# Optimization experiments

Hardware: AMD Instinct MI355X
Metric: run time of the kernel (lower is better)

Reference implementation:

```python
import jax, jax.numpy as jnp
import numpy as np

BS = 128  # quantization block size


def _dequant(w, s, bs):
    # w: [E, O, I]; s: [E, O//bs, I//bs] block scales -> broadcast to full weight
    return w * jnp.repeat(jnp.repeat(s, bs, axis=1), bs, axis=2)


def setup_inputs() -> dict:
    key = jax.random.key(0)
    ks = jax.random.split(key, 9)
    T, H, I, E, K = 512, 2048, 1024, 16, 4
    x = jax.random.normal(ks[0], (T, H), dtype=jnp.float32)
    w0 = jax.random.normal(ks[1], (E, I, H), dtype=jnp.float32) * 0.02
    w1 = jax.random.normal(ks[2], (E, I, H), dtype=jnp.float32) * 0.02
    w2 = jax.random.normal(ks[3], (E, H, I), dtype=jnp.float32) * 0.02
    s0 = jax.random.uniform(ks[4], (E, I // BS, H // BS), dtype=jnp.float32) + 0.5
    s1 = jax.random.uniform(ks[5], (E, I // BS, H // BS), dtype=jnp.float32) + 0.5
    s2 = jax.random.uniform(ks[6], (E, H // BS, I // BS), dtype=jnp.float32) + 0.5
    selected_experts = jax.random.randint(ks[7], (T, K), 0, E, dtype=jnp.int64)
    routing_weights = jax.random.uniform(ks[8], (T, K), dtype=jnp.float32)
    return {"x": x, "w0": w0, "w1": w1, "w2": w2, "s0": s0, "s1": s1,
            "s2": s2, "selected_experts": selected_experts,
            "routing_weights": routing_weights}


def reference(x, w0, w1, w2, s0, s1, s2, selected_experts, routing_weights):
    # Dequantize block-quantized expert weights
    w0d = _dequant(w0, s0, BS)  # [E, I, H] gate proj
    w1d = _dequant(w1, s1, BS)  # [E, I, H] up proj
    w2d = _dequant(w2, s2, BS)  # [E, H, I] down proj
    # SwiGLU FFN for every (token, expert) pair via batched GEMMs
    g = jnp.einsum('th,eih->tei', x, w0d)          # [T, E, I]
    u = jnp.einsum('th,eih->tei', x, w1d)          # [T, E, I]
    h = jax.nn.silu(g) * u                          # [T, E, I]
    y = jnp.einsum('tei,ehi->teh', h, w2d)          # [T, E, H]
    # Gather the top-k selected experts per token and weight them
    idx = selected_experts[:, :, None]              # [T, K, 1]
    y_sel = jnp.take_along_axis(y, idx, axis=1)     # [T, K, H]
    out = y_sel * routing_weights[:, :, None]       # [T, K, H]
    return out
```

## Files before the change

### kernel.cpp

```cpp
#include <hip/hip_runtime.h>
#include <math.h>

#define T_DIM 512
#define H_DIM 2048
#define I_DIM 1024
#define E_DIM 16
#define NP    2048
#define BM    64
#define MAXCH 48
#define LIST_OFF 256
#define HWS_OFF  4096
#define BK    128
#define LDK   136

typedef float  float4v __attribute__((ext_vector_type(4)));
typedef short  short8v __attribute__((ext_vector_type(8)));

__device__ __forceinline__ unsigned int bfr(float f) {
    unsigned int u = __builtin_bit_cast(unsigned int, f);
    return (u + 0x7fffu + ((u >> 16) & 1u)) >> 16;
}
__device__ __forceinline__ unsigned int cvt2(float a, float b) {
    unsigned int r;
    asm("v_cvt_pk_bf16_f32 %0, %1, %2" : "=v"(r) : "v"(a), "v"(b));
    return r;
}

__global__ __launch_bounds__(1024) void route_kernel(const int* __restrict__ sel,
                                                     int* __restrict__ meta) {
    __shared__ int cnt[E_DIM];
    __shared__ int wptr[E_DIM];
    int tid = threadIdx.x;
    if (tid < E_DIM) cnt[tid] = 0;
    __syncthreads();
    int p0 = tid, p1 = tid + 1024;
    int e0 = sel[p0], e1 = sel[p1];
    atomicAdd(&cnt[e0], 1);
    atomicAdd(&cnt[e1], 1);
    for (int i = tid; i < MAXCH * BM; i += 1024) meta[LIST_OFF + i] = -1;
    __syncthreads();
    if (tid == 0) {
        int off = 0, ci = 0;
        for (int e = 0; e < E_DIM; ++e) {
            wptr[e] = off;
            int nch = (cnt[e] + BM - 1) / BM;
            for (int j = 0; j < nch; ++j) meta[32 + ci++] = e;
            off += nch * BM;
        }
        for (; ci < MAXCH; ++ci) meta[32 + ci] = -1;
    }
    __syncthreads();
    int pos0 = atomicAdd(&wptr[e0], 1);
    meta[LIST_OFF + pos0] = p0;
    int pos1 = atomicAdd(&wptr[e1], 1);
    meta[LIST_OFF + pos1] = p1;
}

__global__ __launch_bounds__(512, 4) void gemm01_kernel(
    const float* __restrict__ x, const float* __restrict__ w0g,
    const float* __restrict__ w1g, const float* __restrict__ s0,
    const float* __restrict__ s1, const int* __restrict__ meta,
    unsigned short* __restrict__ hbuf) {
    int e = meta[32 + blockIdx.y];
    if (e < 0) return;
    int itile = blockIdx.x;
    int tid = threadIdx.x;

    __shared__ unsigned short xs[BM][LDK];
    __shared__ unsigned short as[BM][LDK];
    __shared__ unsigned short bs[BM][LDK];
    __shared__ int prow[BM];
    __shared__ int trow[BM];

    if (tid < BM) {
        int p = meta[LIST_OFF + blockIdx.y * BM + tid];
        prow[tid] = p;
        trow[tid] = p >= 0 ? (p >> 2) : 0;
    }
    __syncthreads();

    const int lane = tid & 63;
    const int wid  = tid >> 6;
    const int wm   = wid & 3;
    const int wn   = wid >> 2;
    const int l15  = lane & 15;
    const int kq   = (lane >> 4) * 8;
    const int ib   = itile >> 1;

    float4v zero = {0.f, 0.f, 0.f, 0.f};
    float4v accg[2], accu[2];
    accg[0] = accg[1] = accu[0] = accu[1] = zero;

    const int r  = tid >> 3;
    const int c0 = tid & 7;
    const float* xrow  = x   + (size_t)trow[r] * H_DIM;
    const float* w0row = w0g + ((size_t)e * I_DIM + itile * 64 + r) * H_DIM;
    const float* w1row = w1g + ((size_t)e * I_DIM + itile * 64 + r) * H_DIM;
    const float* s0p = s0 + ((size_t)e * (I_DIM/128) + ib) * (H_DIM/128);
    const float* s1p = s1 + ((size_t)e * (I_DIM/128) + ib) * (H_DIM/128);

    float4 px[4], pa[4], pb[4];
#pragma unroll
    for (int q = 0; q < 4; ++q) {
        int c4 = (c0 + q * 8) * 4;
        px[q] = *(const float4*)(xrow + c4);
        pa[q] = *(const float4*)(w0row + c4);
        pb[q] = *(const float4*)(w1row + c4);
    }

    for (int hb = 0; hb < H_DIM / BK; ++hb) {
        float sg = s0p[hb];
        float su = s1p[hb];
#pragma unroll
        for (int q = 0; q < 4; ++q) {
            int c4 = (c0 + q * 8) * 4;
            *(uint2*)&xs[r][c4] = make_uint2(cvt2(px[q].x, px[q].y), cvt2(px[q].z, px[q].w));
            *(uint2*)&as[r][c4] = make_uint2(cvt2(pa[q].x * sg, pa[q].y * sg),
                                             cvt2(pa[q].z * sg, pa[q].w * sg));
            *(uint2*)&bs[r][c4] = make_uint2(cvt2(pb[q].x * su, pb[q].y * su),
                                             cvt2(pb[q].z * su, pb[q].w * su));
        }
        __syncthreads();
        if (hb + 1 < H_DIM / BK) {
            const int h0 = (hb + 1) * BK;
#pragma unroll
            for (int q = 0; q < 4; ++q) {
                int c4 = (c0 + q * 8) * 4;
                px[q] = *(const float4*)(xrow + h0 + c4);
                pa[q] = *(const float4*)(w0row + h0 + c4);
                pb[q] = *(const float4*)(w1row + h0 + c4);
            }
        }
#pragma unroll
        for (int ks = 0; ks < BK / 32; ++ks) {
            int koff = ks * 32 + kq;
            short8v af = *(const short8v*)&xs[wm * 16 + l15][koff];
#pragma unroll
            for (int nt = 0; nt < 2; ++nt) {
                short8v b0 = *(const short8v*)&as[wn * 32 + nt * 16 + l15][koff];
                accg[nt] = __builtin_amdgcn_mfma_f32_16x16x32_bf16(af, b0, accg[nt], 0, 0, 0);
                short8v b1 = *(const short8v*)&bs[wn * 32 + nt * 16 + l15][koff];
                accu[nt] = __builtin_amdgcn_mfma_f32_16x16x32_bf16(af, b1, accu[nt], 0, 0, 0);
            }
        }
        __syncthreads();
    }

    int rowb = wm * 16 + (lane >> 4) * 4;
    int colb = itile * 64 + wn * 32 + l15;
#pragma unroll
    for (int nt = 0; nt < 2; ++nt) {
#pragma unroll
        for (int rg = 0; rg < 4; ++rg) {
            int p = prow[rowb + rg];
            if (p < 0) continue;
            float g = accg[nt][rg], u = accu[nt][rg];
            float h = g / (1.f + __expf(-g)) * u;
            hbuf[(size_t)p * I_DIM + colb + nt * 16] = (unsigned short)bfr(h);
        }
    }
}

__global__ __launch_bounds__(512, 4) void gemm2_kernel(
    const unsigned short* __restrict__ hbuf, const float* __restrict__ w2g,
    const float* __restrict__ s2, const float* __restrict__ rw,
    const int* __restrict__ meta, float* __restrict__ out) {
    int e = meta[32 + blockIdx.y];
    if (e < 0) return;
    int htile = blockIdx.x;
    int tid = threadIdx.x;

    __shared__ unsigned short hs[BM][LDK];
    __shared__ unsigned short wsm[BM][LDK];
    __shared__ int prow[BM];

    if (tid < BM) prow[tid] = meta[LIST_OFF + blockIdx.y * BM + tid];
    __syncthreads();

    const int lane = tid & 63;
    const int wid  = tid >> 6;
    const int wm   = wid & 3;
    const int wn   = wid >> 2;
    const int l15  = lane & 15;
    const int kq   = (lane >> 4) * 8;
    const int hbk  = htile >> 1;

    float4v zero = {0.f, 0.f, 0.f, 0.f};
    float4v acc[2];
    acc[0] = acc[1] = zero;

    const int r  = tid >> 3;
    const int c0 = tid & 7;
    int pr = prow[r]; if (pr < 0) pr = 0;
    const unsigned short* hrow = hbuf + (size_t)pr * I_DIM;
    const float* wrow = w2g + ((size_t)e * H_DIM + htile * 64 + r) * I_DIM;
    const float* s2p = s2 + ((size_t)e * (H_DIM/128) + hbk) * (I_DIM/128);

    uint2  ph[4];
    float4 pw[4];
#pragma unroll
    for (int q = 0; q < 4; ++q) {
        int c4 = (c0 + q * 8) * 4;
        ph[q] = *(const uint2*)(hrow + c4);
        pw[q] = *(const float4*)(wrow + c4);
    }

    for (int ibk = 0; ibk < I_DIM / BK; ++ibk) {
        float sc = s2p[ibk];
#pragma unroll
        for (int q = 0; q < 4; ++q) {
            int c4 = (c0 + q * 8) * 4;
            *(uint2*)&hs[r][c4] = ph[q];
            *(uint2*)&wsm[r][c4] = make_uint2(cvt2(pw[q].x * sc, pw[q].y * sc),
                                              cvt2(pw[q].z * sc, pw[q].w * sc));
        }
        __syncthreads();
        if (ibk + 1 < I_DIM / BK) {
            const int i0 = (ibk + 1) * BK;
#pragma unroll
            for (int q = 0; q < 4; ++q) {
                int c4 = (c0 + q * 8) * 4;
                ph[q] = *(const uint2*)(hrow + i0 + c4);
                pw[q] = *(const float4*)(wrow + i0 + c4);
            }
        }
#pragma unroll
        for (int ks = 0; ks < BK / 32; ++ks) {
            int koff = ks * 32 + kq;
            short8v af = *(const short8v*)&hs[wm * 16 + l15][koff];
#pragma unroll
            for (int nt = 0; nt < 2; ++nt) {
                short8v bfv = *(const short8v*)&wsm[wn * 32 + nt * 16 + l15][koff];
                acc[nt] = __builtin_amdgcn_mfma_f32_16x16x32_bf16(af, bfv, acc[nt], 0, 0, 0);
            }
        }
        __syncthreads();
    }

    int rowb = wm * 16 + (lane >> 4) * 4;
    int colb = htile * 64 + wn * 32 + l15;
#pragma unroll
    for (int nt = 0; nt < 2; ++nt) {
#pragma unroll
        for (int rg = 0; rg < 4; ++rg) {
            int p = prow[rowb + rg];
            if (p < 0) continue;
            out[(size_t)p * H_DIM + colb + nt * 16] = acc[nt][rg] * rw[p];
        }
    }
}

extern "C" void kernel_launch(void* const* d_in, const int* in_sizes, int n_in,
                              void* d_out, int out_size, void* d_ws, size_t ws_size,
                              hipStream_t stream) {
    const float* x  = (const float*)d_in[0];
    const float* w0 = (const float*)d_in[1];
    const float* w1 = (const float*)d_in[2];
    const float* w2 = (const float*)d_in[3];
    const float* s0 = (const float*)d_in[4];
    const float* s1 = (const float*)d_in[5];
    const float* s2 = (const float*)d_in[6];
    const int* sel  = (const int*)d_in[7];
    const float* rw = (const float*)d_in[8];
    float* out = (float*)d_out;
    int* meta = (int*)d_ws;
    unsigned short* hbuf = (unsigned short*)((float*)d_ws + HWS_OFF);

    route_kernel<<<1, 1024, 0, stream>>>(sel, meta);
    gemm01_kernel<<<dim3(I_DIM / 64, MAXCH), 512, 0, stream>>>(x, w0, w1, s0, s1, meta, hbuf);
    gemm2_kernel<<<dim3(H_DIM / 64, MAXCH), 512, 0, stream>>>(hbuf, w2, s2, rw, meta, out);
}
```

Before: 427.5 us.

## Enlarge routed token chunk to 256 rows with 1024-thread blocks

Each expert chunk now covers 256 routed token rows instead of 64, and each block runs 16 waves, each computing 16 rows by 64 columns. Each weight tile loaded and dequantized from fp32 is therefore reused across four times as many tokens, which cuts redundant weight traffic and per-chunk dequant work in both GEMMs. The cost is more padding waste for experts whose counts do not fill 256 rows, fewer blocks in the grid, and larger shared memory and register use per block, which lowers occupancy.

```diff
diff --git a/kernel.cpp b/kernel.cpp
--- a/kernel.cpp
+++ b/kernel.cpp
@@ -6,10 +6,10 @@
 #define I_DIM 1024
 #define E_DIM 16
 #define NP    2048
-#define BM    64
-#define MAXCH 48
+#define PM    256
+#define MAXCH 24
 #define LIST_OFF 256
-#define HWS_OFF  4096
+#define HWS_OFF  8192
 #define BK    128
 #define LDK   136
 
@@ -37,15 +37,15 @@
     int e0 = sel[p0], e1 = sel[p1];
     atomicAdd(&cnt[e0], 1);
     atomicAdd(&cnt[e1], 1);
-    for (int i = tid; i < MAXCH * BM; i += 1024) meta[LIST_OFF + i] = -1;
+    for (int i = tid; i < MAXCH * PM; i += 1024) meta[LIST_OFF + i] = -1;
     __syncthreads();
     if (tid == 0) {
         int off = 0, ci = 0;
         for (int e = 0; e < E_DIM; ++e) {
             wptr[e] = off;
-            int nch = (cnt[e] + BM - 1) / BM;
+            int nch = (cnt[e] + PM - 1) / PM;
             for (int j = 0; j < nch; ++j) meta[32 + ci++] = e;
-            off += nch * BM;
+            off += nch * PM;
         }
         for (; ci < MAXCH; ++ci) meta[32 + ci] = -1;
     }
@@ -56,7 +56,7 @@
     meta[LIST_OFF + pos1] = p1;
 }
 
-__global__ __launch_bounds__(512, 4) void gemm01_kernel(
+__global__ __launch_bounds__(1024, 4) void gemm01_kernel(
     const float* __restrict__ x, const float* __restrict__ w0g,
     const float* __restrict__ w1g, const float* __restrict__ s0,
     const float* __restrict__ s1, const int* __restrict__ meta,
@@ -66,14 +66,14 @@
     int itile = blockIdx.x;
     int tid = threadIdx.x;
 
-    __shared__ unsigned short xs[BM][LDK];
-    __shared__ unsigned short as[BM][LDK];
-    __shared__ unsigned short bs[BM][LDK];
-    __shared__ int prow[BM];
-    __shared__ int trow[BM];
-
-    if (tid < BM) {
-        int p = meta[LIST_OFF + blockIdx.y * BM + tid];
+    __shared__ unsigned short xs[PM][LDK];
+    __shared__ unsigned short as[64][LDK];
+    __shared__ unsigned short bs[64][LDK];
+    __shared__ int prow[PM];
+    __shared__ int trow[PM];
+
+    if (tid < PM) {
+        int p = meta[LIST_OFF + blockIdx.y * PM + tid];
         prow[tid] = p;
         trow[tid] = p >= 0 ? (p >> 2) : 0;
     }
@@ -81,75 +81,77 @@
 
     const int lane = tid & 63;
     const int wid  = tid >> 6;
-    const int wm   = wid & 3;
-    const int wn   = wid >> 2;
     const int l15  = lane & 15;
     const int kq   = (lane >> 4) * 8;
     const int ib   = itile >> 1;
 
     float4v zero = {0.f, 0.f, 0.f, 0.f};
-    float4v accg[2], accu[2];
-    accg[0] = accg[1] = accu[0] = accu[1] = zero;
-
-    const int r  = tid >> 3;
-    const int c0 = tid & 7;
-    const float* xrow  = x   + (size_t)trow[r] * H_DIM;
-    const float* w0row = w0g + ((size_t)e * I_DIM + itile * 64 + r) * H_DIM;
-    const float* w1row = w1g + ((size_t)e * I_DIM + itile * 64 + r) * H_DIM;
+    float4v accg[4], accu[4];
+#pragma unroll
+    for (int t = 0; t < 4; ++t) { accg[t] = zero; accu[t] = zero; }
+
+    const int rx = tid >> 2, cx = tid & 3;
+    const int rw_ = tid >> 4, cw = tid & 15;
+    const float* xrow  = x   + (size_t)trow[rx] * H_DIM + cx * 32;
+    const float* w0row = w0g + ((size_t)e * I_DIM + itile * 64 + rw_) * H_DIM + cw * 8;
+    const float* w1row = w1g + ((size_t)e * I_DIM + itile * 64 + rw_) * H_DIM + cw * 8;
     const float* s0p = s0 + ((size_t)e * (I_DIM/128) + ib) * (H_DIM/128);
     const float* s1p = s1 + ((size_t)e * (I_DIM/128) + ib) * (H_DIM/128);
 
-    float4 px[4], pa[4], pb[4];
-#pragma unroll
-    for (int q = 0; q < 4; ++q) {
-        int c4 = (c0 + q * 8) * 4;
-        px[q] = *(const float4*)(xrow + c4);
-        pa[q] = *(const float4*)(w0row + c4);
-        pb[q] = *(const float4*)(w1row + c4);
-    }
+    float4 px[8], pa0, pa1, pb0, pb1;
+#pragma unroll
+    for (int q = 0; q < 8; ++q) px[q] = *(const float4*)(xrow + q * 4);
+    pa0 = *(const float4*)(w0row);
+    pa1 = *(const float4*)(w0row + 4);
+    pb0 = *(const float4*)(w1row);
+    pb1 = *(const float4*)(w1row + 4);
 
     for (int hb = 0; hb < H_DIM / BK; ++hb) {
         float sg = s0p[hb];
         float su = s1p[hb];
 #pragma unroll
-        for (int q = 0; q < 4; ++q) {
-            int c4 = (c0 + q * 8) * 4;
-            *(uint2*)&xs[r][c4] = make_uint2(cvt2(px[q].x, px[q].y), cvt2(px[q].z, px[q].w));
-            *(uint2*)&as[r][c4] = make_uint2(cvt2(pa[q].x * sg, pa[q].y * sg),
-                                             cvt2(pa[q].z * sg, pa[q].w * sg));
-            *(uint2*)&bs[r][c4] = make_uint2(cvt2(pb[q].x * su, pb[q].y * su),
-                                             cvt2(pb[q].z * su, pb[q].w * su));
-        }
+        for (int j = 0; j < 4; ++j) {
+            uint4 v = make_uint4(cvt2(px[2*j].x,   px[2*j].y),
+                                 cvt2(px[2*j].z,   px[2*j].w),
+                                 cvt2(px[2*j+1].x, px[2*j+1].y),
+                                 cvt2(px[2*j+1].z, px[2*j+1].w));
+            *(uint4*)&xs[rx][cx * 32 + j * 8] = v;
+        }
+        *(uint4*)&as[rw_][cw * 8] = make_uint4(
+            cvt2(pa0.x * sg, pa0.y * sg), cvt2(pa0.z * sg, pa0.w * sg),
+            cvt2(pa1.x * sg, pa1.y * sg), cvt2(pa1.z * sg, pa1.w * sg));
+        *(uint4*)&bs[rw_][cw * 8] = make_uint4(
+            cvt2(pb0.x * su, pb0.y * su), cvt2(pb0.z * su, pb0.w * su),
+            cvt2(pb1.x * su, pb1.y * su), cvt2(pb1.z * su, pb1.w * su));
         __syncthreads();
         if (hb + 1 < H_DIM / BK) {
             const int h0 = (hb + 1) * BK;
 #pragma unroll
-            for (int q = 0; q < 4; ++q) {
-                int c4 = (c0 + q * 8) * 4;
-                px[q] = *(const float4*)(xrow + h0 + c4);
-                pa[q] = *(const float4*)(w0row + h0 + c4);
-                pb[q] = *(const float4*)(w1row + h0 + c4);
-            }
+            for (int q = 0; q < 8; ++q) px[q] = *(const float4*)(xrow + h0 + q * 4);
+            pa0 = *(const float4*)(w0row + h0);
+            pa1 = *(const float4*)(w0row + h0 + 4);
+            pb0 = *(const float4*)(w1row + h0);
+            pb1 = *(const float4*)(w1row + h0 + 4);
         }
 #pragma unroll
         for (int ks = 0; ks < BK / 32; ++ks) {
             int koff = ks * 32 + kq;
-            short8v af = *(const short8v*)&xs[wm * 16 + l15][koff];
-#pragma unroll
-            for (int nt = 0; nt < 2; ++nt) {
-                short8v b0 = *(const short8v*)&as[wn * 32 + nt * 16 + l15][koff];
+            short8v af = *(const short8v*)&xs[wid * 16 + l15][koff];
+#pragma unroll
+            for (int nt = 0; nt < 4; ++nt) {
+                short8v b0 = *(const short8v*)&as[nt * 16 + l15][koff];
                 accg[nt] = __builtin_amdgcn_mfma_f32_16x16x32_bf16(af, b0, accg[nt], 0, 0, 0);
-                short8v b1 = *(const short8v*)&bs[wn * 32 + nt * 16 + l15][koff];
+                short8v b1 = *(const short8v*)&bs[nt * 16 + l15][koff];
                 accu[nt] = __builtin_amdgcn_mfma_f32_16x16x32_bf16(af, b1, accu[nt], 0, 0, 0);
             }
         }
         __syncthreads();
     }
 
-    int rowb = wm * 16 + (lane >> 4) * 4;
-    int colb = itile * 64 + wn * 32 + l15;
-#pragma unroll
-    for (int nt = 0; nt < 2; ++nt) {
+    int rowb = wid * 16 + (lane >> 4) * 4;
+    int colb = itile * 64 + l15;
+#pragma unroll
+    for (int nt = 0; nt < 4; ++nt) {
 #pragma unroll
         for (int rg = 0; rg < 4; ++rg) {
             int p = prow[rowb + rg];
@@ -161,7 +163,7 @@
     }
 }
 
-__global__ __launch_bounds__(512, 4) void gemm2_kernel(
+__global__ __launch_bounds__(1024, 4) void gemm2_kernel(
     const unsigned short* __restrict__ hbuf, const float* __restrict__ w2g,
     const float* __restrict__ s2, const float* __restrict__ rw,
     const int* __restrict__ meta, float* __restrict__ out) {
@@ -170,77 +172,77 @@
     int htile = blockIdx.x;
     int tid = threadIdx.x;
 
-    __shared__ unsigned short hs[BM][LDK];
-    __shared__ unsigned short wsm[BM][LDK];
-    __shared__ int prow[BM];
-
-    if (tid < BM) prow[tid] = meta[LIST_OFF + blockIdx.y * BM + tid];
+    __shared__ unsigned short hs[PM][LDK];
+    __shared__ unsigned short wsm[64][LDK];
+    __shared__ int prow[PM];
+
+    if (tid < PM) prow[tid] = meta[LIST_OFF + blockIdx.y * PM + tid];
     __syncthreads();
 
     const int lane = tid & 63;
     const int wid  = tid >> 6;
-    const int wm   = wid & 3;
-    const int wn   = wid >> 2;
     const int l15  = lane & 15;
     const int kq   = (lane >> 4) * 8;
     const int hbk  = htile >> 1;
 
     float4v zero = {0.f, 0.f, 0.f, 0.f};
-    float4v acc[2];
-    acc[0] = acc[1] = zero;
-
-    const int r  = tid >> 3;
-    const int c0 = tid & 7;
-    int pr = prow[r]; if (pr < 0) pr = 0;
-    const unsigned short* hrow = hbuf + (size_t)pr * I_DIM;
-    const float* wrow = w2g + ((size_t)e * H_DIM + htile * 64 + r) * I_DIM;
+    float4v acc[4];
+#pragma unroll
+    for (int t = 0; t < 4; ++t) acc[t] = zero;
+
+    const int rx = tid >> 2, cx = tid & 3;
+    const int rw_ = tid >> 4, cw = tid & 15;
+    int pr = prow[rx]; if (pr < 0) pr = 0;
+    const unsigned short* hrow = hbuf + (size_t)pr * I_DIM + cx * 32;
+    const float* wrow = w2g + ((size_t)e * H_DIM + htile * 64 + rw_) * I_DIM + cw * 8;
     const float* s2p = s2 + ((size_t)e * (H_DIM/128) + hbk) * (I_DIM/128);
 
-    uint2  ph[4];
-    float4 pw[4];
-#pragma unroll
-    for (int q = 0; q < 4; ++q) {
-        int c4 = (c0 + q * 8) * 4;
-        ph[q] = *(const uint2*)(hrow + c4);
-        pw[q] = *(const float4*)(wrow + c4);
-    }
+    uint4  ph[2];
+    float4 pw0, pw1;
+    ph[0] = *(const uint4*)(hrow);
+    ph[1] = *(const uint4*)(hrow + 8);
+    uint4 ph2[2];
+    ph2[0] = *(const uint4*)(hrow + 16);
+    ph2[1] = *(const uint4*)(hrow + 24);
+    pw0 = *(const float4*)(wrow);
+    pw1 = *(const float4*)(wrow + 4);
 
     for (int ibk = 0; ibk < I_DIM / BK; ++ibk) {
         float sc = s2p[ibk];
-#pragma unroll
-        for (int q = 0; q < 4; ++q) {
-            int c4 = (c0 + q * 8) * 4;
-            *(uint2*)&hs[r][c4] = ph[q];
-            *(uint2*)&wsm[r][c4] = make_uint2(cvt2(pw[q].x * sc, pw[q].y * sc),
-                                              cvt2(pw[q].z * sc, pw[q].w * sc));
-        }
+        *(uint4*)&hs[rx][cx * 32]      = ph[0];
+        *(uint4*)&hs[rx][cx * 32 + 8]  = ph[1];
+        *(uint4*)&hs[rx][cx * 32 + 16] = ph2[0];
+        *(uint4*)&hs[rx][cx * 32 + 24] = ph2[1];
+        *(uint4*)&wsm[rw_][cw * 8] = make_uint4(
+            cvt2(pw0.x * sc, pw0.y * sc), cvt2(pw0.z * sc, pw0.w * sc),
+            cvt2(pw1.x * sc, pw1.y * sc), cvt2(pw1.z * sc, pw1.w * sc));
         __syncthreads();
         if (ibk + 1 < I_DIM / BK) {
             const int i0 = (ibk + 1) * BK;
-#pragma unroll
-            for (int q = 0; q < 4; ++q) {
-                int c4 = (c0 + q * 8) * 4;
-                ph[q] = *(const uint2*)(hrow + i0 + c4);
-                pw[q] = *(const float4*)(wrow + i0 + c4);
-            }
+            ph[0]  = *(const uint4*)(hrow + i0);
+            ph[1]  = *(const uint4*)(hrow + i0 + 8);
+            ph2[0] = *(const uint4*)(hrow + i0 + 16);
+            ph2[1] = *(const uint4*)(hrow + i0 + 24);
+            pw0 = *(const float4*)(wrow + i0);
+            pw1 = *(const float4*)(wrow + i0 + 4);
         }
 #pragma unroll
         for (int ks = 0; ks < BK / 32; ++ks) {
             int koff = ks * 32 + kq;
-            short8v af = *(const short8v*)&hs[wm * 16 + l15][koff];
-#pragma unroll
-            for (int nt = 0; nt < 2; ++nt) {
-                short8v bfv = *(const short8v*)&wsm[wn * 32 + nt * 16 + l15][koff];
+            short8v af = *(const short8v*)&hs[wid * 16 + l15][koff];
+#pragma unroll
+            for (int nt = 0; nt < 4; ++nt) {
+                short8v bfv = *(const short8v*)&wsm[nt * 16 + l15][koff];
                 acc[nt] = __builtin_amdgcn_mfma_f32_16x16x32_bf16(af, bfv, acc[nt], 0, 0, 0);
             }
         }
         __syncthreads();
     }
 
-    int rowb = wm * 16 + (lane >> 4) * 4;
-    int colb = htile * 64 + wn * 32 + l15;
-#pragma unroll
-    for (int nt = 0; nt < 2; ++nt) {
+    int rowb = wid * 16 + (lane >> 4) * 4;
+    int colb = htile * 64 + l15;
+#pragma unroll
+    for (int nt = 0; nt < 4; ++nt) {
 #pragma unroll
         for (int rg = 0; rg < 4; ++rg) {
             int p = prow[rowb + rg];
@@ -267,6 +269,6 @@
     unsigned short* hbuf = (unsigned short*)((float*)d_ws + HWS_OFF);
 
     route_kernel<<<1, 1024, 0, stream>>>(sel, meta);
-    gemm01_kernel<<<dim3(I_DIM / 64, MAXCH), 512, 0, stream>>>(x, w0, w1, s0, s1, meta, hbuf);
-    gemm2_kernel<<<dim3(H_DIM / 64, MAXCH), 512, 0, stream>>>(hbuf, w2, s2, rw, meta, out);
-}
+    gemm01_kernel<<<dim3(I_DIM / 64, MAXCH), 1024, 0, stream>>>(x, w0, w1, s0, s1, meta, hbuf);
+    gemm2_kernel<<<dim3(H_DIM / 64, MAXCH), 1024, 0, stream>>>(hbuf, w2, s2, rw, meta, out);
+}
```

Result: slower. 447.1 us (+4.6%).
